# Kernel tuning notes

Hardware: AMD Instinct MI355X
Metric: run time of the kernel (lower is better)

## Reference

```python
import jax, jax.numpy as jnp
import numpy as np

MODES = 256


def setup_inputs() -> dict:
    key = jax.random.key(0)
    k1, k2, k3, k4, k5 = jax.random.split(key, 5)
    B, C_IN, C_OUT, N, KM = 8, 128, 128, 8192, 32
    scale = 1.0 / (C_IN * C_OUT)
    return {
        "x": jax.random.normal(k1, (B, C_IN, N), dtype=jnp.float32),
        "wbases": jax.random.normal(k2, (B, N, MODES), dtype=jnp.float32),
        "bases": jax.random.normal(k3, (B, N, MODES), dtype=jnp.float32),
        "weights": scale * jax.random.normal(k4, (C_IN, C_OUT, KM), dtype=jnp.float32),
        "D": jax.random.normal(k5, (KM, MODES), dtype=jnp.float32),
    }


def reference(x, wbases, bases, weights, D):
    # Project onto weighted bases: (b, c_in, n) x (b, n, modes) -> (b, c_in, modes)
    x_hat = jnp.einsum('bcx,bxk->bck', x, wbases[:, :, :MODES])
    # D-weighted channel mixing. Original: x_hat1[b,i,j,k] = x_hat[b,i,k]*D[j,k];
    # y[b,o,k] = sum_{i,j} x_hat1[b,i,j,k] * weights[i,o,j]
    # Equivalent fused contraction (same math, no 4D broadcast):
    y_hat = jnp.einsum('bik,jk,ioj->bok', x_hat, D, weights)
    # Reconstruct on output bases: (b, c_out, modes) x (b, n, modes) -> (b, c_out, n)
    y = jnp.einsum('bck,bxk->bcx', y_hat, bases[:, :, :MODES])
    return y
```

## Files before the change

### kernel.cpp

```cpp
#include <hip/hip_runtime.h>

#define B_    8
#define CIN   128
#define COUT  128
#define NX    8192
#define KMJ   32
#define MODES 256

typedef short bf16x8 __attribute__((ext_vector_type(8)));
typedef float f32x4  __attribute__((ext_vector_type(4)));

__device__ __forceinline__ float bf2f(unsigned short u) {
    union { unsigned int i; float f; } v; v.i = ((unsigned int)u) << 16; return v.f;
}
__device__ __forceinline__ unsigned short f2bf(float f) {
    union { float f; unsigned int i; } v; v.f = f;
    unsigned int x = v.i;
    return (unsigned short)((x + 0x7fffu + ((x >> 16) & 1u)) >> 16);
}
__device__ __forceinline__ bf16x8 cvt8(const float* __restrict__ p) {
    f32x4 a = *(const f32x4*)p;
    f32x4 b = *(const f32x4*)(p + 4);
    bf16x8 r;
    r[0] = (short)f2bf(a[0]); r[1] = (short)f2bf(a[1]);
    r[2] = (short)f2bf(a[2]); r[3] = (short)f2bf(a[3]);
    r[4] = (short)f2bf(b[0]); r[5] = (short)f2bf(b[1]);
    r[6] = (short)f2bf(b[2]); r[7] = (short)f2bf(b[3]);
    return r;
}
__device__ __forceinline__ ushort4 cvt4(f32x4 a) {
    ushort4 r;
    r.x = f2bf(a[0]); r.y = f2bf(a[1]); r.z = f2bf(a[2]); r.w = f2bf(a[3]);
    return r;
}

__global__ __launch_bounds__(256) void k1_wk(const float* __restrict__ W,
                                             const float* __restrict__ D,
                                             unsigned short* __restrict__ Wk) {
    int wave = threadIdx.x >> 6, lane = threadIdx.x & 63;
    int quad = lane >> 4, l16 = lane & 15;
    int gw  = blockIdx.x * 4 + wave;
    int oi0 = gw * 16;
    int i0  = oi0 & 127, o0 = oi0 >> 7;
    bf16x8 bfrag = cvt8(W + ((size_t)(i0 + l16) * COUT + o0) * KMJ + quad * 8);
    for (int mt = 0; mt < 16; mt++) {
        int k0 = mt * 16;
        bf16x8 afrag;
#pragma unroll
        for (int jj = 0; jj < 8; jj++)
            afrag[jj] = (short)f2bf(D[(quad * 8 + jj) * MODES + k0 + l16]);
        f32x4 acc = {0.f, 0.f, 0.f, 0.f};
        acc = __builtin_amdgcn_mfma_f32_16x16x32_bf16(afrag, bfrag, acc, 0, 0, 0);
#pragma unroll
        for (int r = 0; r < 4; r++)
            Wk[(size_t)(k0 + quad * 4 + r) * (CIN * COUT) + oi0 + l16] = f2bf(acc[r]);
    }
}

__global__ __launch_bounds__(512) void k2_xhat(const float* __restrict__ X,
                                               const float* __restrict__ WB,
                                               unsigned short* __restrict__ PART) {
    __shared__ __align__(16) unsigned short Xs[128 * 40];
    __shared__ __align__(16) unsigned short WBs[32 * 260];
    int nt = blockIdx.x, b = blockIdx.y;
    int r0 = nt * 256;
    int t  = threadIdx.x;
    int wave = t >> 6, lane = t & 63;
    int wm = wave >> 2, wn = wave & 3;
    int quad = lane >> 4, l16 = lane & 15;

    const float* xb  = X  + (size_t)b * CIN * NX;
    const float* wbb = WB + (size_t)b * NX * MODES;

    int xn4 = t & 7,  xc  = t >> 3;
    int wk4 = t & 63, wn0 = t >> 6;

    f32x4 acc[4][4];
#pragma unroll
    for (int i = 0; i < 4; i++)
#pragma unroll
        for (int j = 0; j < 4; j++) acc[i][j] = (f32x4){0.f, 0.f, 0.f, 0.f};

    for (int s = 0; s < 8; s++) {
        int rs = r0 + s * 32;
        f32x4 xv0 = *(const f32x4*)(xb + (size_t)xc * NX + rs + xn4 * 4);
        f32x4 xv1 = *(const f32x4*)(xb + (size_t)(xc + 64) * NX + rs + xn4 * 4);
        f32x4 wv[4];
#pragma unroll
        for (int r = 0; r < 4; r++)
            wv[r] = *(const f32x4*)(wbb + (size_t)(rs + wn0 + 8 * r) * MODES + wk4 * 4);

        __syncthreads();
        *(ushort4*)(Xs + xc * 40 + xn4 * 4)        = cvt4(xv0);
        *(ushort4*)(Xs + (xc + 64) * 40 + xn4 * 4) = cvt4(xv1);
#pragma unroll
        for (int r = 0; r < 4; r++)
            *(ushort4*)(WBs + (wn0 + 8 * r) * 260 + wk4 * 4) = cvt4(wv[r]);
        __syncthreads();

        bf16x8 af[4];
#pragma unroll
        for (int tm = 0; tm < 4; tm++)
            af[tm] = *(const bf16x8*)(Xs + (wm * 64 + tm * 16 + l16) * 40 + quad * 8);
        bf16x8 bfv[4];
#pragma unroll
        for (int tn = 0; tn < 4; tn++) {
            int km = wn * 64 + tn * 16 + l16;
#pragma unroll
            for (int jj = 0; jj < 8; jj++)
                bfv[tn][jj] = (short)WBs[(quad * 8 + jj) * 260 + km];
        }
#pragma unroll
        for (int tm = 0; tm < 4; tm++)
#pragma unroll
            for (int tn = 0; tn < 4; tn++)
                acc[tm][tn] = __builtin_amdgcn_mfma_f32_16x16x32_bf16(af[tm], bfv[tn], acc[tm][tn], 0, 0, 0);
    }

    unsigned short* pb = PART + ((size_t)b * 32 + nt) * (CIN * MODES);
#pragma unroll
    for (int tm = 0; tm < 4; tm++) {
        int c = wm * 64 + tm * 16 + quad * 4;
#pragma unroll
        for (int tn = 0; tn < 4; tn++) {
            int km = wn * 64 + tn * 16 + l16;
#pragma unroll
            for (int r = 0; r < 4; r++)
                pb[(size_t)(c + r) * MODES + km] = f2bf(acc[tm][tn][r]);
        }
    }
}

__global__ __launch_bounds__(256) void k2b_red(const unsigned short* __restrict__ PART,
                                               float* __restrict__ XH) {
    int e0 = blockIdx.x * 1024 + threadIdx.x;
#pragma unroll
    for (int r = 0; r < 4; r++) {
        int e = e0 + r * 256;
        int b = e >> 15, rem = e & 32767;
        const unsigned short* p = PART + (size_t)b * 32 * (CIN * MODES) + rem;
        float acc = 0.f;
#pragma unroll
        for (int nt = 0; nt < 32; nt++) acc += bf2f(p[nt * (CIN * MODES)]);
        XH[e] = acc;
    }
}

__global__ __launch_bounds__(256) void k3_yhat(const float* __restrict__ XH,
                                               const unsigned short* __restrict__ Wk,
                                               unsigned short* __restrict__ YH) {
    __shared__ float xs[128][8];
    int k = blockIdx.x;
    int t = threadIdx.x;
#pragma unroll
    for (int l = 0; l < 4; l++) {
        int e = l * 256 + t;
        int i = e >> 3, b = e & 7;
        xs[i][b] = XH[(size_t)b * (CIN * MODES) + (size_t)i * MODES + k];
    }
    __syncthreads();
    int o = t & 127, bh = t >> 7;
    const unsigned short* wp = Wk + (size_t)k * (CIN * COUT) + (size_t)o * CIN;
    f32x4 acc = {0.f, 0.f, 0.f, 0.f};
    for (int ii = 0; ii < 16; ii++) {
        bf16x8 wc = *(const bf16x8*)(wp + ii * 8);
#pragma unroll
        for (int jj = 0; jj < 8; jj++) {
            float w = bf2f((unsigned short)wc[jj]);
            f32x4 xv = *(const f32x4*)&xs[ii * 8 + jj][bh * 4];
            acc += w * xv;
        }
    }
#pragma unroll
    for (int r = 0; r < 4; r++)
        YH[((size_t)(bh * 4 + r) * COUT + o) * MODES + k] = f2bf(acc[r]);
}

__global__ __launch_bounds__(256) void k4_y(const unsigned short* __restrict__ YH,
                                            const float* __restrict__ BA,
                                            float* __restrict__ Y) {
    __shared__ __align__(16) unsigned short As[128 * 32];
    __shared__ __align__(16) unsigned short Bs[128 * 32];
    int b  = blockIdx.y;
    int n0 = blockIdx.x * 128;
    int t  = threadIdx.x;
    int wave = t >> 6, lane = t & 63;
    int wm = wave >> 1, wn = wave & 1;
    int quad = lane >> 4, l16 = lane & 15;

    const unsigned short* yhb = YH + (size_t)b * COUT * MODES;
    const float* bab = BA + (size_t)b * NX * MODES + (size_t)n0 * MODES;

    int E0 = t * 8;
    int row0 = E0 >> 5, kk0 = E0 & 31;
    int row1 = (2048 + E0) >> 5, kk1 = (2048 + E0) & 31;

    f32x4 acc[4][4];
#pragma unroll
    for (int i = 0; i < 4; i++)
#pragma unroll
        for (int j = 0; j < 4; j++) acc[i][j] = (f32x4){0.f, 0.f, 0.f, 0.f};

    bf16x8 av0 = *(const bf16x8*)(yhb + (size_t)row0 * MODES + kk0);
    bf16x8 av1 = *(const bf16x8*)(yhb + (size_t)row1 * MODES + kk1);
    f32x4 bv0a = *(const f32x4*)(bab + (size_t)row0 * MODES + kk0);
    f32x4 bv0b = *(const f32x4*)(bab + (size_t)row0 * MODES + kk0 + 4);
    f32x4 bv1a = *(const f32x4*)(bab + (size_t)row1 * MODES + kk1);
    f32x4 bv1b = *(const f32x4*)(bab + (size_t)row1 * MODES + kk1 + 4);

    for (int step = 0; step < 8; step++) {
        __syncthreads();
        *(bf16x8*)(As + E0)        = av0;
        *(bf16x8*)(As + 2048 + E0) = av1;
        bf16x8 bs0, bs1;
        bs0[0]=(short)f2bf(bv0a[0]); bs0[1]=(short)f2bf(bv0a[1]);
        bs0[2]=(short)f2bf(bv0a[2]); bs0[3]=(short)f2bf(bv0a[3]);
        bs0[4]=(short)f2bf(bv0b[0]); bs0[5]=(short)f2bf(bv0b[1]);
        bs0[6]=(short)f2bf(bv0b[2]); bs0[7]=(short)f2bf(bv0b[3]);
        bs1[0]=(short)f2bf(bv1a[0]); bs1[1]=(short)f2bf(bv1a[1]);
        bs1[2]=(short)f2bf(bv1a[2]); bs1[3]=(short)f2bf(bv1a[3]);
        bs1[4]=(short)f2bf(bv1b[0]); bs1[5]=(short)f2bf(bv1b[1]);
        bs1[6]=(short)f2bf(bv1b[2]); bs1[7]=(short)f2bf(bv1b[3]);
        *(bf16x8*)(Bs + E0)        = bs0;
        *(bf16x8*)(Bs + 2048 + E0) = bs1;
        __syncthreads();

        if (step < 7) {
            int ks = (step + 1) * 32;
            av0  = *(const bf16x8*)(yhb + (size_t)row0 * MODES + ks + kk0);
            av1  = *(const bf16x8*)(yhb + (size_t)row1 * MODES + ks + kk1);
            bv0a = *(const f32x4*)(bab + (size_t)row0 * MODES + ks + kk0);
            bv0b = *(const f32x4*)(bab + (size_t)row0 * MODES + ks + kk0 + 4);
            bv1a = *(const f32x4*)(bab + (size_t)row1 * MODES + ks + kk1);
            bv1b = *(const f32x4*)(bab + (size_t)row1 * MODES + ks + kk1 + 4);
        }

        bf16x8 af[4], bfv[4];
#pragma unroll
        for (int tm = 0; tm < 4; tm++) {
            int c = wm * 64 + tm * 16 + l16;
            af[tm] = *(const bf16x8*)(As + c * 32 + quad * 8);
        }
#pragma unroll
        for (int tn = 0; tn < 4; tn++) {
            int n = wn * 64 + tn * 16 + l16;
            bfv[tn] = *(const bf16x8*)(Bs + n * 32 + quad * 8);
        }
#pragma unroll
        for (int tm = 0; tm < 4; tm++)
#pragma unroll
            for (int tn = 0; tn < 4; tn++)
                acc[tm][tn] = __builtin_amdgcn_mfma_f32_16x16x32_bf16(af[tm], bfv[tn], acc[tm][tn], 0, 0, 0);
    }

    float* yb = Y + (size_t)b * COUT * NX;
#pragma unroll
    for (int tm = 0; tm < 4; tm++) {
        int o = wm * 64 + tm * 16 + quad * 4;
#pragma unroll
        for (int tn = 0; tn < 4; tn++) {
            int n = n0 + wn * 64 + tn * 16 + l16;
#pragma unroll
            for (int r = 0; r < 4; r++)
                yb[(size_t)(o + r) * NX + n] = acc[tm][tn][r];
        }
    }
}

extern "C" void kernel_launch(void* const* d_in, const int* in_sizes, int n_in,
                              void* d_out, int out_size, void* d_ws, size_t ws_size,
                              hipStream_t stream) {
    const float* X  = (const float*)d_in[0];
    const float* WB = (const float*)d_in[1];
    const float* BA = (const float*)d_in[2];
    const float* W  = (const float*)d_in[3];
    const float* D  = (const float*)d_in[4];
    float* Y = (float*)d_out;

    char* ws = (char*)d_ws;
    unsigned short* Wk   = (unsigned short*)ws;
    float*          XH   = (float*)(ws + (8u << 20));
    unsigned short* YH   = (unsigned short*)(ws + (9u << 20));
    unsigned short* PART = (unsigned short*)(ws + (10u << 20));

    k1_wk  <<<256,          256, 0, stream>>>(W, D, Wk);
    k2_xhat<<<dim3(32, 8),  512, 0, stream>>>(X, WB, PART);
    k2b_red<<<256,          256, 0, stream>>>(PART, XH);
    k3_yhat<<<MODES,        256, 0, stream>>>(XH, Wk, YH);
    k4_y   <<<dim3(64, 8),  256, 0, stream>>>(YH, BA, Y);
}
```

Baseline: 220.3 us.

## Split GEMM kernels into smaller tiles for more blocks across CUs

The x_hat projection kernel now tiles the mode dimension into four 64-wide slices and runs 256-thread blocks, giving four times as many blocks. The y_hat mixing kernel splits output channels across four blocks, one output per thread. The reconstruction kernel halves the N tile to 64 and pads its shared-memory rows to 36 to reduce bank conflicts, but drops the register prefetch of the next K slice. The aim is better occupancy and CU coverage on a 256-CU part. The cost is more redundant loads of X and YH per block and less load/compute overlap in the last kernel.

```diff
diff --git a/kernel.cpp b/kernel.cpp
--- a/kernel.cpp
+++ b/kernel.cpp
@@ -57,73 +57,75 @@
     }
 }
 
-__global__ __launch_bounds__(512) void k2_xhat(const float* __restrict__ X,
+__global__ __launch_bounds__(256) void k2_xhat(const float* __restrict__ X,
                                                const float* __restrict__ WB,
                                                unsigned short* __restrict__ PART) {
     __shared__ __align__(16) unsigned short Xs[128 * 40];
-    __shared__ __align__(16) unsigned short WBs[32 * 260];
-    int nt = blockIdx.x, b = blockIdx.y;
+    __shared__ __align__(16) unsigned short WBs[32 * 68];
+    int nt = blockIdx.x, kt = blockIdx.y, b = blockIdx.z;
     int r0 = nt * 256;
     int t  = threadIdx.x;
     int wave = t >> 6, lane = t & 63;
-    int wm = wave >> 2, wn = wave & 3;
+    int wm = wave >> 1, wn = wave & 1;
     int quad = lane >> 4, l16 = lane & 15;
 
     const float* xb  = X  + (size_t)b * CIN * NX;
-    const float* wbb = WB + (size_t)b * NX * MODES;
+    const float* wbb = WB + (size_t)b * NX * MODES + kt * 64;
 
     int xn4 = t & 7,  xc  = t >> 3;
-    int wk4 = t & 63, wn0 = t >> 6;
-
-    f32x4 acc[4][4];
+    int wk4 = t & 15, wn0 = t >> 4;
+
+    f32x4 acc[4][2];
 #pragma unroll
     for (int i = 0; i < 4; i++)
 #pragma unroll
-        for (int j = 0; j < 4; j++) acc[i][j] = (f32x4){0.f, 0.f, 0.f, 0.f};
+        for (int j = 0; j < 2; j++) acc[i][j] = (f32x4){0.f, 0.f, 0.f, 0.f};
 
     for (int s = 0; s < 8; s++) {
         int rs = r0 + s * 32;
-        f32x4 xv0 = *(const f32x4*)(xb + (size_t)xc * NX + rs + xn4 * 4);
-        f32x4 xv1 = *(const f32x4*)(xb + (size_t)(xc + 64) * NX + rs + xn4 * 4);
-        f32x4 wv[4];
+        f32x4 xv[4], wv[2];
 #pragma unroll
         for (int r = 0; r < 4; r++)
-            wv[r] = *(const f32x4*)(wbb + (size_t)(rs + wn0 + 8 * r) * MODES + wk4 * 4);
-
-        __syncthreads();
-        *(ushort4*)(Xs + xc * 40 + xn4 * 4)        = cvt4(xv0);
-        *(ushort4*)(Xs + (xc + 64) * 40 + xn4 * 4) = cvt4(xv1);
+            xv[r] = *(const f32x4*)(xb + (size_t)(xc + 32 * r) * NX + rs + xn4 * 4);
+#pragma unroll
+        for (int r = 0; r < 2; r++)
+            wv[r] = *(const f32x4*)(wbb + (size_t)(rs + wn0 + 16 * r) * MODES + wk4 * 4);
+
+        __syncthreads();
 #pragma unroll
         for (int r = 0; r < 4; r++)
-            *(ushort4*)(WBs + (wn0 + 8 * r) * 260 + wk4 * 4) = cvt4(wv[r]);
+            *(ushort4*)(Xs + (xc + 32 * r) * 40 + xn4 * 4) = cvt4(xv[r]);
+#pragma unroll
+        for (int r = 0; r < 2; r++)
+            *(ushort4*)(WBs + (wn0 + 16 * r) * 68 + wk4 * 4) = cvt4(wv[r]);
         __syncthreads();
 
         bf16x8 af[4];
 #pragma unroll
         for (int tm = 0; tm < 4; tm++)
             af[tm] = *(const bf16x8*)(Xs + (wm * 64 + tm * 16 + l16) * 40 + quad * 8);
-        bf16x8 bfv[4];
-#pragma unroll
-        for (int tn = 0; tn < 4; tn++) {
-            int km = wn * 64 + tn * 16 + l16;
+        bf16x8 bfv[2];
+#pragma unroll
+        for (int tn = 0; tn < 2; tn++) {
+            int km = wn * 32 + tn * 16 + l16;
 #pragma unroll
             for (int jj = 0; jj < 8; jj++)
-                bfv[tn][jj] = (short)WBs[(quad * 8 + jj) * 260 + km];
+                bfv[tn][jj] = (short)WBs[(quad * 8 + jj) * 68 + km];
         }
 #pragma unroll
         for (int tm = 0; tm < 4; tm++)
 #pragma unroll
-            for (int tn = 0; tn < 4; tn++)
+            for (int tn = 0; tn < 2; tn++)
                 acc[tm][tn] = __builtin_amdgcn_mfma_f32_16x16x32_bf16(af[tm], bfv[tn], acc[tm][tn], 0, 0, 0);
     }
 
-    unsigned short* pb = PART + ((size_t)b * 32 + nt) * (CIN * MODES);
+    unsigned short* pb = PART + ((size_t)b * 32 + nt) * (CIN * MODES) + kt * 64;
 #pragma unroll
     for (int tm = 0; tm < 4; tm++) {
         int c = wm * 64 + tm * 16 + quad * 4;
 #pragma unroll
-        for (int tn = 0; tn < 4; tn++) {
-            int km = wn * 64 + tn * 16 + l16;
+        for (int tn = 0; tn < 2; tn++) {
+            int km = wn * 32 + tn * 16 + l16;
 #pragma unroll
             for (int r = 0; r < 4; r++)
                 pb[(size_t)(c + r) * MODES + km] = f2bf(acc[tm][tn][r]);
@@ -150,7 +152,7 @@
                                                const unsigned short* __restrict__ Wk,
                                                unsigned short* __restrict__ YH) {
     __shared__ float xs[128][8];
-    int k = blockIdx.x;
+    int k = blockIdx.x, oc = blockIdx.y;
     int t = threadIdx.x;
 #pragma unroll
     for (int l = 0; l < 4; l++) {
@@ -159,30 +161,26 @@
         xs[i][b] = XH[(size_t)b * (CIN * MODES) + (size_t)i * MODES + k];
     }
     __syncthreads();
-    int o = t & 127, bh = t >> 7;
+    int o = oc * 32 + (t >> 3), b = t & 7;
     const unsigned short* wp = Wk + (size_t)k * (CIN * COUT) + (size_t)o * CIN;
-    f32x4 acc = {0.f, 0.f, 0.f, 0.f};
+    float acc = 0.f;
+#pragma unroll 4
     for (int ii = 0; ii < 16; ii++) {
         bf16x8 wc = *(const bf16x8*)(wp + ii * 8);
 #pragma unroll
-        for (int jj = 0; jj < 8; jj++) {
-            float w = bf2f((unsigned short)wc[jj]);
-            f32x4 xv = *(const f32x4*)&xs[ii * 8 + jj][bh * 4];
-            acc += w * xv;
-        }
-    }
-#pragma unroll
-    for (int r = 0; r < 4; r++)
-        YH[((size_t)(bh * 4 + r) * COUT + o) * MODES + k] = f2bf(acc[r]);
+        for (int jj = 0; jj < 8; jj++)
+            acc += bf2f((unsigned short)wc[jj]) * xs[ii * 8 + jj][b];
+    }
+    YH[((size_t)b * COUT + o) * MODES + k] = f2bf(acc);
 }
 
 __global__ __launch_bounds__(256) void k4_y(const unsigned short* __restrict__ YH,
                                             const float* __restrict__ BA,
                                             float* __restrict__ Y) {
-    __shared__ __align__(16) unsigned short As[128 * 32];
-    __shared__ __align__(16) unsigned short Bs[128 * 32];
-    int b  = blockIdx.y;
-    int n0 = blockIdx.x * 128;
+    __shared__ __align__(16) unsigned short As[128 * 36];
+    __shared__ __align__(16) unsigned short Bs[64 * 36];
+    int nt = blockIdx.x, b = blockIdx.y;
+    int n0 = nt * 64;
     int t  = threadIdx.x;
     int wave = t >> 6, lane = t & 63;
     int wm = wave >> 1, wn = wave & 1;
@@ -191,65 +189,45 @@
     const unsigned short* yhb = YH + (size_t)b * COUT * MODES;
     const float* bab = BA + (size_t)b * NX * MODES + (size_t)n0 * MODES;
 
-    int E0 = t * 8;
-    int row0 = E0 >> 5, kk0 = E0 & 31;
-    int row1 = (2048 + E0) >> 5, kk1 = (2048 + E0) & 31;
-
-    f32x4 acc[4][4];
+    int E0  = t * 8;
+    int ar0 = E0 >> 5, akk = E0 & 31;
+    int ar1 = (2048 + E0) >> 5;
+    int bk4 = t & 7, bn = t >> 3;
+
+    f32x4 acc[4][2];
 #pragma unroll
     for (int i = 0; i < 4; i++)
 #pragma unroll
-        for (int j = 0; j < 4; j++) acc[i][j] = (f32x4){0.f, 0.f, 0.f, 0.f};
-
-    bf16x8 av0 = *(const bf16x8*)(yhb + (size_t)row0 * MODES + kk0);
-    bf16x8 av1 = *(const bf16x8*)(yhb + (size_t)row1 * MODES + kk1);
-    f32x4 bv0a = *(const f32x4*)(bab + (size_t)row0 * MODES + kk0);
-    f32x4 bv0b = *(const f32x4*)(bab + (size_t)row0 * MODES + kk0 + 4);
-    f32x4 bv1a = *(const f32x4*)(bab + (size_t)row1 * MODES + kk1);
-    f32x4 bv1b = *(const f32x4*)(bab + (size_t)row1 * MODES + kk1 + 4);
+        for (int j = 0; j < 2; j++) acc[i][j] = (f32x4){0.f, 0.f, 0.f, 0.f};
 
     for (int step = 0; step < 8; step++) {
-        __syncthreads();
-        *(bf16x8*)(As + E0)        = av0;
-        *(bf16x8*)(As + 2048 + E0) = av1;
-        bf16x8 bs0, bs1;
-        bs0[0]=(short)f2bf(bv0a[0]); bs0[1]=(short)f2bf(bv0a[1]);
-        bs0[2]=(short)f2bf(bv0a[2]); bs0[3]=(short)f2bf(bv0a[3]);
-        bs0[4]=(short)f2bf(bv0b[0]); bs0[5]=(short)f2bf(bv0b[1]);
-        bs0[6]=(short)f2bf(bv0b[2]); bs0[7]=(short)f2bf(bv0b[3]);
-        bs1[0]=(short)f2bf(bv1a[0]); bs1[1]=(short)f2bf(bv1a[1]);
-        bs1[2]=(short)f2bf(bv1a[2]); bs1[3]=(short)f2bf(bv1a[3]);
-        bs1[4]=(short)f2bf(bv1b[0]); bs1[5]=(short)f2bf(bv1b[1]);
-        bs1[6]=(short)f2bf(bv1b[2]); bs1[7]=(short)f2bf(bv1b[3]);
-        *(bf16x8*)(Bs + E0)        = bs0;
-        *(bf16x8*)(Bs + 2048 + E0) = bs1;
-        __syncthreads();
-
-        if (step < 7) {
-            int ks = (step + 1) * 32;
-            av0  = *(const bf16x8*)(yhb + (size_t)row0 * MODES + ks + kk0);
-            av1  = *(const bf16x8*)(yhb + (size_t)row1 * MODES + ks + kk1);
-            bv0a = *(const f32x4*)(bab + (size_t)row0 * MODES + ks + kk0);
-            bv0b = *(const f32x4*)(bab + (size_t)row0 * MODES + ks + kk0 + 4);
-            bv1a = *(const f32x4*)(bab + (size_t)row1 * MODES + ks + kk1);
-            bv1b = *(const f32x4*)(bab + (size_t)row1 * MODES + ks + kk1 + 4);
-        }
-
-        bf16x8 af[4], bfv[4];
-#pragma unroll
-        for (int tm = 0; tm < 4; tm++) {
-            int c = wm * 64 + tm * 16 + l16;
-            af[tm] = *(const bf16x8*)(As + c * 32 + quad * 8);
-        }
-#pragma unroll
-        for (int tn = 0; tn < 4; tn++) {
-            int n = wn * 64 + tn * 16 + l16;
-            bfv[tn] = *(const bf16x8*)(Bs + n * 32 + quad * 8);
-        }
-#pragma unroll
-        for (int tm = 0; tm < 4; tm++)
-#pragma unroll
-            for (int tn = 0; tn < 4; tn++)
+        int ks = step * 32;
+        bf16x8 av0 = *(const bf16x8*)(yhb + (size_t)ar0 * MODES + ks + akk);
+        bf16x8 av1 = *(const bf16x8*)(yhb + (size_t)ar1 * MODES + ks + akk);
+        f32x4 bv[2];
+#pragma unroll
+        for (int r = 0; r < 2; r++)
+            bv[r] = *(const f32x4*)(bab + (size_t)(bn + 32 * r) * MODES + ks + bk4 * 4);
+
+        __syncthreads();
+        *(bf16x8*)(As + ar0 * 36 + akk) = av0;
+        *(bf16x8*)(As + ar1 * 36 + akk) = av1;
+#pragma unroll
+        for (int r = 0; r < 2; r++)
+            *(ushort4*)(Bs + (bn + 32 * r) * 36 + bk4 * 4) = cvt4(bv[r]);
+        __syncthreads();
+
+        bf16x8 af[4], bfv[2];
+#pragma unroll
+        for (int tm = 0; tm < 4; tm++)
+            af[tm] = *(const bf16x8*)(As + (wm * 64 + tm * 16 + l16) * 36 + quad * 8);
+#pragma unroll
+        for (int tn = 0; tn < 2; tn++)
+            bfv[tn] = *(const bf16x8*)(Bs + (wn * 32 + tn * 16 + l16) * 36 + quad * 8);
+#pragma unroll
+        for (int tm = 0; tm < 4; tm++)
+#pragma unroll
+            for (int tn = 0; tn < 2; tn++)
                 acc[tm][tn] = __builtin_amdgcn_mfma_f32_16x16x32_bf16(af[tm], bfv[tn], acc[tm][tn], 0, 0, 0);
     }
 
@@ -258,8 +236,8 @@
     for (int tm = 0; tm < 4; tm++) {
         int o = wm * 64 + tm * 16 + quad * 4;
 #pragma unroll
-        for (int tn = 0; tn < 4; tn++) {
-            int n = n0 + wn * 64 + tn * 16 + l16;
+        for (int tn = 0; tn < 2; tn++) {
+            int n = n0 + wn * 32 + tn * 16 + l16;
 #pragma unroll
             for (int r = 0; r < 4; r++)
                 yb[(size_t)(o + r) * NX + n] = acc[tm][tn][r];
@@ -283,9 +261,9 @@
     unsigned short* YH   = (unsigned short*)(ws + (9u << 20));
     unsigned short* PART = (unsigned short*)(ws + (10u << 20));
 
-    k1_wk  <<<256,          256, 0, stream>>>(W, D, Wk);
-    k2_xhat<<<dim3(32, 8),  512, 0, stream>>>(X, WB, PART);
-    k2b_red<<<256,          256, 0, stream>>>(PART, XH);
-    k3_yhat<<<MODES,        256, 0, stream>>>(XH, Wk, YH);
-    k4_y   <<<dim3(64, 8),  256, 0, stream>>>(YH, BA, Y);
-}
+    k1_wk  <<<256,             256, 0, stream>>>(W, D, Wk);
+    k2_xhat<<<dim3(32, 4, 8),  256, 0, stream>>>(X, WB, PART);
+    k2b_red<<<256,             256, 0, stream>>>(PART, XH);
+    k3_yhat<<<dim3(256, 4),    256, 0, stream>>>(XH, Wk, YH);
+    k4_y   <<<dim3(128, 8),    256, 0, stream>>>(YH, BA, Y);
+}
```

Result: slower. 232.6 us (+5.6%).
